# Kernel tuning notes

Hardware: AMD Instinct MI355X
Metric: run time of the kernel (lower is better)

## Reference

```python
import jax, jax.numpy as jnp
import numpy as np

LN_EPS = 1e-5

def setup_inputs() -> dict:
    key = jax.random.key(0)
    k1, k2, k3, k4, k5, k6 = jax.random.split(key, 6)
    N, D, E_DIM = 100000, 512, 512
    M, n_edges = 500000, 100000
    z_nodes = jax.random.normal(k1, (N, D), dtype=jnp.float32)
    member_idx = jax.random.randint(k2, (M,), 0, N, dtype=jnp.int32)
    seg_ids = jnp.sort(jax.random.randint(k3, (M,), 0, n_edges, dtype=jnp.int32))
    # aggregator params: Linear(D -> E_DIM), LayerNorm(E_DIM)
    W = jax.random.normal(k4, (D, E_DIM), dtype=jnp.float32) / np.sqrt(D)
    b = jax.random.normal(k5, (E_DIM,), dtype=jnp.float32) * 0.01
    gamma = jnp.ones((E_DIM,), dtype=jnp.float32)
    beta = jnp.zeros((E_DIM,), dtype=jnp.float32)
    return {"z_nodes": z_nodes, "W": W, "b": b, "gamma": gamma, "beta": beta,
            "member_idx": member_idx, "seg_ids": seg_ids, "n_edges": n_edges}

def reference(z_nodes, W, b, gamma, beta, member_idx, seg_ids, n_edges):
    # ragged gather + per-edge mean pool (segment mean)
    gathered = z_nodes[member_idx]                                   # [M, D]
    sums = jax.ops.segment_sum(gathered, seg_ids, num_segments=n_edges)  # [E, D]
    counts = jax.ops.segment_sum(jnp.ones((member_idx.shape[0],), dtype=z_nodes.dtype),
                                 seg_ids, num_segments=n_edges)      # [E]
    mean = sums / jnp.maximum(counts, 1.0)[:, None]                  # [E, D]
    # Linear -> LayerNorm -> GELU (torch GELU default is exact erf form)
    h = mean @ W + b                                                 # [E, edge_dim]
    mu = jnp.mean(h, axis=-1, keepdims=True)
    var = jnp.mean(jnp.square(h - mu), axis=-1, keepdims=True)
    h = (h - mu) * jax.lax.rsqrt(var + LN_EPS) * gamma + beta
    return jax.nn.gelu(h, approximate=False)
```

## Files before the change

### kernel.cpp

```cpp
#include <hip/hip_runtime.h>
#include <hip/hip_bf16.h>
#include <stdint.h>


typedef __attribute__((ext_vector_type(8))) short short8;
typedef __attribute__((ext_vector_type(4))) float f32x4;
typedef __attribute__((ext_vector_type(4))) float float4v;
typedef __attribute__((ext_vector_type(4))) unsigned short u16x4;

__device__ __forceinline__ unsigned short f2bf(float f) {
  __hip_bfloat16 h = __float2bfloat16(f);
  return __builtin_bit_cast(unsigned short, h);
}
__device__ __forceinline__ float bf2f(unsigned short u) {
  __hip_bfloat16 h = __builtin_bit_cast(__hip_bfloat16, u);
  return __bfloat162float(h);
}

__device__ __forceinline__ void gld_lds16(const void* g, void* l) {
  __builtin_amdgcn_global_load_lds(
      (const __attribute__((address_space(1))) uint32_t*)g,
      (__attribute__((address_space(3))) uint32_t*)l, 16, 0, 0);
}

__global__ void k_zero(int* __restrict__ beg, int* __restrict__ end_, int E) {
  int i = blockIdx.x * 256 + threadIdx.x;
  if (i < E) { beg[i] = 0; end_[i] = 0; }
}

__global__ void k_bounds(const int* __restrict__ seg, int* __restrict__ beg,
                         int* __restrict__ end_, int M) {
  int i = blockIdx.x * 256 + threadIdx.x;
  if (i >= M) return;
  int s = seg[i];
  if (i == 0 || seg[i - 1] != s) beg[s] = i;
  if (i == M - 1 || seg[i + 1] != s) end_[s] = i + 1;
}

__global__ void k_wsplit(const float* __restrict__ W, unsigned short* __restrict__ Whi,
                         unsigned short* __restrict__ Wlo) {
  int t = blockIdx.x * 256 + threadIdx.x;
  if (t >= 512 * 512) return;
  int k = t >> 9, c = t & 511;
  float w = W[t];
  unsigned short hi = f2bf(w);
  unsigned short lo = f2bf(w - bf2f(hi));
  int o = (k >> 3) * 4096 + c * 8 + (k & 7);
  Whi[o] = hi;
  Wlo[o] = lo;
}

__global__ void k_mean(const float* __restrict__ z, const int* __restrict__ midx,
                       const int* __restrict__ beg, const int* __restrict__ end_,
                       unsigned short* a16) {
  const int e = blockIdx.x;
  const int t = threadIdx.x;
  const int b = beg[e], en = end_[e];
  float4v acc = {0.f, 0.f, 0.f, 0.f};
  for (int m = b; m < en; ++m) {
    const int r = midx[m];
    const float4v v = *(const float4v*)(z + (size_t)r * 512 + t * 4);
    acc.x += v.x; acc.y += v.y; acc.z += v.z; acc.w += v.w;
  }
  const int cnt = en - b;
  const float den = (float)(cnt > 0 ? cnt : 1);
  float m0 = acc.x / den, m1 = acc.y / den, m2 = acc.z / den, m3 = acc.w / den;
  u16x4 hi, lo;
  hi.x = f2bf(m0); lo.x = f2bf(m0 - bf2f(hi.x));
  hi.y = f2bf(m1); lo.y = f2bf(m1 - bf2f(hi.y));
  hi.z = f2bf(m2); lo.z = f2bf(m2 - bf2f(hi.z));
  hi.w = f2bf(m3); lo.w = f2bf(m3 - bf2f(hi.w));
  *(u16x4*)(a16 + (size_t)e * 1024 + t * 4) = hi;
  *(u16x4*)(a16 + (size_t)e * 1024 + 512 + t * 4) = lo;
}

#define KSTEPS 48

__launch_bounds__(256, 2)
__global__ void k_gemm(const unsigned short* a16,
                       const unsigned short* __restrict__ Whi,
                       const unsigned short* __restrict__ Wlo,
                       const float* __restrict__ bias, const float* __restrict__ gamma,
                       const float* __restrict__ beta, float* out, int E) {
  __shared__ short lA[2][64 * 32];
  __shared__ short lB[2][4 * 512 * 8];
  __shared__ float lRed[64 * 4];
  __shared__ float lMu[64], lRs[64];

  const int t = threadIdx.x;
  const int w = t >> 6, l = t & 63;
  const int g = l >> 4, l15 = l & 15;
  const int cw = w * 128;
  const int e0 = blockIdx.x * 64;

  f32x4 acc[4][8];
#pragma unroll
  for (int mf = 0; mf < 4; ++mf)
#pragma unroll
    for (int nf = 0; nf < 8; ++nf) acc[mf][nf] = (f32x4){0.f, 0.f, 0.f, 0.f};

  auto stage = [&](int s) {
    const int p = s >> 4, kt = s & 15, buf = s & 1;
    const int poff = (p == 1) ? 512 : 0;
    const unsigned short* Bs = (p == 2) ? Wlo : Whi;
    {
      const int row = t >> 2, cd = t & 3;
      const int cs = cd ^ ((row >> 1) & 3);
      int rsrc = e0 + row;
      if (rsrc > E - 1) rsrc = E - 1;
      gld_lds16(a16 + (size_t)rsrc * 1024 + poff + kt * 32 + cs * 8,
                &lA[buf][w * 512]);
    }
    const unsigned short* gb = Bs + (size_t)kt * 16384;
#pragma unroll
    for (int i = 0; i < 8; ++i) {
      gld_lds16(gb + (size_t)(i * 256 + t) * 8, &lB[buf][(i * 256 + w * 64) * 8]);
    }
  };

  stage(0);
  for (int s = 0; s < KSTEPS; ++s) {
    __syncthreads();
    if (s + 1 < KSTEPS) stage(s + 1);
    const int buf = s & 1;
    short8 af[4];
#pragma unroll
    for (int mf = 0; mf < 4; ++mf) {
      const int R = 16 * mf + l15;
      const int cc = g ^ ((R >> 1) & 3);
      af[mf] = *(const short8*)&lA[buf][R * 32 + cc * 8];
    }
#pragma unroll
    for (int nf = 0; nf < 8; ++nf) {
      const short8 bf = *(const short8*)&lB[buf][(g * 512 + cw + 16 * nf + l15) * 8];
#pragma unroll
      for (int mf = 0; mf < 4; ++mf)
        acc[mf][nf] = __builtin_amdgcn_mfma_f32_16x16x32_bf16(af[mf], bf, acc[mf][nf], 0, 0, 0);
    }
  }
  __syncthreads();

  float bia[8], gam[8], bet[8];
#pragma unroll
  for (int nf = 0; nf < 8; ++nf) {
    const int col = cw + 16 * nf + l15;
    bia[nf] = bias[col]; gam[nf] = gamma[col]; bet[nf] = beta[col];
  }
#pragma unroll
  for (int mf = 0; mf < 4; ++mf)
#pragma unroll
    for (int nf = 0; nf < 8; ++nf)
#pragma unroll
      for (int r = 0; r < 4; ++r) acc[mf][nf][r] += bia[nf];

  float s_[4][4];
#pragma unroll
  for (int mf = 0; mf < 4; ++mf)
#pragma unroll
    for (int r = 0; r < 4; ++r) {
      float v = 0.f;
#pragma unroll
      for (int nf = 0; nf < 8; ++nf) v += acc[mf][nf][r];
      v += __shfl_xor(v, 1); v += __shfl_xor(v, 2);
      v += __shfl_xor(v, 4); v += __shfl_xor(v, 8);
      s_[mf][r] = v;
    }
  if (l15 == 0) {
#pragma unroll
    for (int mf = 0; mf < 4; ++mf)
#pragma unroll
      for (int r = 0; r < 4; ++r) lRed[(16 * mf + 4 * g + r) * 4 + w] = s_[mf][r];
  }
  __syncthreads();
  if (t < 64) lMu[t] = (lRed[t * 4] + lRed[t * 4 + 1] + lRed[t * 4 + 2] + lRed[t * 4 + 3]) * (1.f / 512.f);
  __syncthreads();

  float mu_[4][4];
#pragma unroll
  for (int mf = 0; mf < 4; ++mf)
#pragma unroll
    for (int r = 0; r < 4; ++r) mu_[mf][r] = lMu[16 * mf + 4 * g + r];
#pragma unroll
  for (int mf = 0; mf < 4; ++mf)
#pragma unroll
    for (int r = 0; r < 4; ++r) {
      float v = 0.f;
#pragma unroll
      for (int nf = 0; nf < 8; ++nf) {
        const float d = acc[mf][nf][r] - mu_[mf][r];
        v += d * d;
      }
      v += __shfl_xor(v, 1); v += __shfl_xor(v, 2);
      v += __shfl_xor(v, 4); v += __shfl_xor(v, 8);
      s_[mf][r] = v;
    }
  if (l15 == 0) {
#pragma unroll
    for (int mf = 0; mf < 4; ++mf)
#pragma unroll
      for (int r = 0; r < 4; ++r) lRed[(16 * mf + 4 * g + r) * 4 + w] = s_[mf][r];
  }
  __syncthreads();
  if (t < 64) {
    const float sse = lRed[t * 4] + lRed[t * 4 + 1] + lRed[t * 4 + 2] + lRed[t * 4 + 3];
    lRs[t] = rsqrtf(sse * (1.f / 512.f) + 1e-5f);
  }
  __syncthreads();

#pragma unroll
  for (int mf = 0; mf < 4; ++mf)
#pragma unroll
    for (int r = 0; r < 4; ++r) {
      const int row = 16 * mf + 4 * g + r;
      const int er = e0 + row;
      if (er >= E) continue;
      const float mu = lMu[row], rs = lRs[row];
#pragma unroll
      for (int nf = 0; nf < 8; ++nf) {
        const int col = cw + 16 * nf + l15;
        const float x = (acc[mf][nf][r] - mu) * rs * gam[nf] + bet[nf];
        const float y = 0.5f * x * (1.f + erff(x * 0.70710678118654752f));
        out[(size_t)er * 512 + col] = y;
      }
    }
}

extern "C" void kernel_launch(void* const* d_in, const int* in_sizes, int n_in,
                              void* d_out, int out_size, void* d_ws, size_t ws_size,
                              hipStream_t stream) {
  const float* z = (const float*)d_in[0];
  const float* W = (const float*)d_in[1];
  const float* bias = (const float*)d_in[2];
  const float* gamma = (const float*)d_in[3];
  const float* beta = (const float*)d_in[4];
  const int* midx = (const int*)d_in[5];
  const int* seg = (const int*)d_in[6];
  const int M = in_sizes[5];
  const int E = out_size / 512;

  char* ws = (char*)d_ws;
  size_t off = 0;
  auto alloc = [&](size_t bytes) {
    void* p = ws + off;
    off = (off + bytes + 255) & ~(size_t)255;
    return p;
  };
  int* beg = (int*)alloc((size_t)E * 4);
  int* end_ = (int*)alloc((size_t)E * 4);
  unsigned short* Whi = (unsigned short*)alloc((size_t)512 * 512 * 2);
  unsigned short* Wlo = (unsigned short*)alloc((size_t)512 * 512 * 2);
  (void)ws_size; (void)n_in;

  unsigned short* a16 = (unsigned short*)d_out;

  k_zero<<<(E + 255) / 256, 256, 0, stream>>>(beg, end_, E);
  k_bounds<<<(M + 255) / 256, 256, 0, stream>>>(seg, beg, end_, M);
  k_wsplit<<<(512 * 512 + 255) / 256, 256, 0, stream>>>(W, Whi, Wlo);
  k_mean<<<E, 128, 0, stream>>>(z, midx, beg, end_, a16);
  k_gemm<<<(E + 63) / 64, 256, 0, stream>>>(a16, Whi, Wlo, bias, gamma, beta,
                                            (float*)d_out, E);
}
```

Before: 803.6 us.

## Unroll gather in mean kernel and load GEMM operands directly from global

The mean kernel now gives each edge one wavefront, handles four members per iteration with two float4 loads per lane, and multiplies by a reciprocal instead of dividing. This is meant to keep more gather loads in flight. The GEMM drops its LDS double-buffered staging and reads A and B fragments straight from global/L2 into registers, removing barriers and LDS traffic. The cost is that operand reuse through shared memory is lost, so B is fetched separately by every wave and block and more cache bandwidth is needed.

```diff
diff --git a/kernel.cpp b/kernel.cpp
--- a/kernel.cpp
+++ b/kernel.cpp
@@ -5,7 +5,6 @@
 
 typedef __attribute__((ext_vector_type(8))) short short8;
 typedef __attribute__((ext_vector_type(4))) float f32x4;
-typedef __attribute__((ext_vector_type(4))) float float4v;
 typedef __attribute__((ext_vector_type(4))) unsigned short u16x4;
 
 __device__ __forceinline__ unsigned short f2bf(float f) {
@@ -15,12 +14,6 @@
 __device__ __forceinline__ float bf2f(unsigned short u) {
   __hip_bfloat16 h = __builtin_bit_cast(__hip_bfloat16, u);
   return __bfloat162float(h);
-}
-
-__device__ __forceinline__ void gld_lds16(const void* g, void* l) {
-  __builtin_amdgcn_global_load_lds(
-      (const __attribute__((address_space(1))) uint32_t*)g,
-      (__attribute__((address_space(3))) uint32_t*)l, 16, 0, 0);
 }
 
 __global__ void k_zero(int* __restrict__ beg, int* __restrict__ end_, int E) {
@@ -52,29 +45,47 @@
 
 __global__ void k_mean(const float* __restrict__ z, const int* __restrict__ midx,
                        const int* __restrict__ beg, const int* __restrict__ end_,
-                       unsigned short* a16) {
-  const int e = blockIdx.x;
-  const int t = threadIdx.x;
+                       unsigned short* a16, int E) {
+  const int w = threadIdx.x >> 6, l = threadIdx.x & 63;
+  const int e = blockIdx.x * 4 + w;
+  if (e >= E) return;
   const int b = beg[e], en = end_[e];
-  float4v acc = {0.f, 0.f, 0.f, 0.f};
-  for (int m = b; m < en; ++m) {
+  const float* zl = z + l * 4;
+  f32x4 a0 = {0.f, 0.f, 0.f, 0.f}, a1 = {0.f, 0.f, 0.f, 0.f};
+  int m = b;
+  for (; m + 4 <= en; m += 4) {
+    const int r0 = midx[m], r1 = midx[m + 1], r2 = midx[m + 2], r3 = midx[m + 3];
+    const f32x4 u0 = *(const f32x4*)(zl + (size_t)r0 * 512);
+    const f32x4 u1 = *(const f32x4*)(zl + (size_t)r0 * 512 + 256);
+    const f32x4 v0 = *(const f32x4*)(zl + (size_t)r1 * 512);
+    const f32x4 v1 = *(const f32x4*)(zl + (size_t)r1 * 512 + 256);
+    const f32x4 s0 = *(const f32x4*)(zl + (size_t)r2 * 512);
+    const f32x4 s1 = *(const f32x4*)(zl + (size_t)r2 * 512 + 256);
+    const f32x4 t0 = *(const f32x4*)(zl + (size_t)r3 * 512);
+    const f32x4 t1 = *(const f32x4*)(zl + (size_t)r3 * 512 + 256);
+    a0 += u0; a1 += u1; a0 += v0; a1 += v1;
+    a0 += s0; a1 += s1; a0 += t0; a1 += t1;
+  }
+  for (; m < en; ++m) {
     const int r = midx[m];
-    const float4v v = *(const float4v*)(z + (size_t)r * 512 + t * 4);
-    acc.x += v.x; acc.y += v.y; acc.z += v.z; acc.w += v.w;
+    a0 += *(const f32x4*)(zl + (size_t)r * 512);
+    a1 += *(const f32x4*)(zl + (size_t)r * 512 + 256);
   }
   const int cnt = en - b;
-  const float den = (float)(cnt > 0 ? cnt : 1);
-  float m0 = acc.x / den, m1 = acc.y / den, m2 = acc.z / den, m3 = acc.w / den;
-  u16x4 hi, lo;
-  hi.x = f2bf(m0); lo.x = f2bf(m0 - bf2f(hi.x));
-  hi.y = f2bf(m1); lo.y = f2bf(m1 - bf2f(hi.y));
-  hi.z = f2bf(m2); lo.z = f2bf(m2 - bf2f(hi.z));
-  hi.w = f2bf(m3); lo.w = f2bf(m3 - bf2f(hi.w));
-  *(u16x4*)(a16 + (size_t)e * 1024 + t * 4) = hi;
-  *(u16x4*)(a16 + (size_t)e * 1024 + 512 + t * 4) = lo;
-}
-
-#define KSTEPS 48
+  const float den = 1.f / (float)(cnt > 0 ? cnt : 1);
+  u16x4 h0, l0, h1, l1;
+#pragma unroll
+  for (int j = 0; j < 4; ++j) {
+    const float m0 = a0[j] * den, m1 = a1[j] * den;
+    h0[j] = f2bf(m0); l0[j] = f2bf(m0 - bf2f(h0[j]));
+    h1[j] = f2bf(m1); l1[j] = f2bf(m1 - bf2f(h1[j]));
+  }
+  unsigned short* rowp = a16 + (size_t)e * 1024;
+  *(u16x4*)(rowp + l * 4) = h0;
+  *(u16x4*)(rowp + 256 + l * 4) = h1;
+  *(u16x4*)(rowp + 512 + l * 4) = l0;
+  *(u16x4*)(rowp + 768 + l * 4) = l1;
+}
 
 __launch_bounds__(256, 2)
 __global__ void k_gemm(const unsigned short* a16,
@@ -82,8 +93,6 @@
                        const unsigned short* __restrict__ Wlo,
                        const float* __restrict__ bias, const float* __restrict__ gamma,
                        const float* __restrict__ beta, float* out, int E) {
-  __shared__ short lA[2][64 * 32];
-  __shared__ short lB[2][4 * 512 * 8];
   __shared__ float lRed[64 * 4];
   __shared__ float lMu[64], lRs[64];
 
@@ -93,52 +102,41 @@
   const int cw = w * 128;
   const int e0 = blockIdx.x * 64;
 
+  const unsigned short* pA[4];
+#pragma unroll
+  for (int mf = 0; mf < 4; ++mf) {
+    int R = e0 + 16 * mf + l15;
+    if (R > E - 1) R = E - 1;
+    pA[mf] = a16 + (size_t)R * 1024 + g * 8;
+  }
+  const size_t bOff = (size_t)g * 4096 + (size_t)(cw + l15) * 8;
+
   f32x4 acc[4][8];
 #pragma unroll
   for (int mf = 0; mf < 4; ++mf)
 #pragma unroll
     for (int nf = 0; nf < 8; ++nf) acc[mf][nf] = (f32x4){0.f, 0.f, 0.f, 0.f};
 
-  auto stage = [&](int s) {
-    const int p = s >> 4, kt = s & 15, buf = s & 1;
+  for (int p = 0; p < 3; ++p) {
+    const unsigned short* pB = ((p == 2) ? Wlo : Whi) + bOff;
     const int poff = (p == 1) ? 512 : 0;
-    const unsigned short* Bs = (p == 2) ? Wlo : Whi;
-    {
-      const int row = t >> 2, cd = t & 3;
-      const int cs = cd ^ ((row >> 1) & 3);
-      int rsrc = e0 + row;
-      if (rsrc > E - 1) rsrc = E - 1;
-      gld_lds16(a16 + (size_t)rsrc * 1024 + poff + kt * 32 + cs * 8,
-                &lA[buf][w * 512]);
-    }
-    const unsigned short* gb = Bs + (size_t)kt * 16384;
-#pragma unroll
-    for (int i = 0; i < 8; ++i) {
-      gld_lds16(gb + (size_t)(i * 256 + t) * 8, &lB[buf][(i * 256 + w * 64) * 8]);
-    }
-  };
-
-  stage(0);
-  for (int s = 0; s < KSTEPS; ++s) {
-    __syncthreads();
-    if (s + 1 < KSTEPS) stage(s + 1);
-    const int buf = s & 1;
-    short8 af[4];
-#pragma unroll
-    for (int mf = 0; mf < 4; ++mf) {
-      const int R = 16 * mf + l15;
-      const int cc = g ^ ((R >> 1) & 3);
-      af[mf] = *(const short8*)&lA[buf][R * 32 + cc * 8];
-    }
-#pragma unroll
-    for (int nf = 0; nf < 8; ++nf) {
-      const short8 bf = *(const short8*)&lB[buf][(g * 512 + cw + 16 * nf + l15) * 8];
+#pragma unroll 2
+    for (int kt = 0; kt < 16; ++kt) {
+      short8 af[4];
 #pragma unroll
       for (int mf = 0; mf < 4; ++mf)
-        acc[mf][nf] = __builtin_amdgcn_mfma_f32_16x16x32_bf16(af[mf], bf, acc[mf][nf], 0, 0, 0);
-    }
-  }
-  __syncthreads();
+        af[mf] = *(const short8*)(pA[mf] + poff + kt * 32);
+      short8 bf[8];
+#pragma unroll
+      for (int nf = 0; nf < 8; ++nf)
+        bf[nf] = *(const short8*)(pB + (size_t)kt * 16384 + nf * 128);
+#pragma unroll
+      for (int nf = 0; nf < 8; ++nf)
+#pragma unroll
+        for (int mf = 0; mf < 4; ++mf)
+          acc[mf][nf] = __builtin_amdgcn_mfma_f32_16x16x32_bf16(af[mf], bf[nf], acc[mf][nf], 0, 0, 0);
+    }
+  }
 
   float bia[8], gam[8], bet[8];
 #pragma unroll
@@ -256,7 +254,7 @@
   k_zero<<<(E + 255) / 256, 256, 0, stream>>>(beg, end_, E);
   k_bounds<<<(M + 255) / 256, 256, 0, stream>>>(seg, beg, end_, M);
   k_wsplit<<<(512 * 512 + 255) / 256, 256, 0, stream>>>(W, Whi, Wlo);
-  k_mean<<<E, 128, 0, stream>>>(z, midx, beg, end_, a16);
+  k_mean<<<(E + 3) / 4, 256, 0, stream>>>(z, midx, beg, end_, a16, E);
   k_gemm<<<(E + 63) / 64, 256, 0, stream>>>(a16, Whi, Wlo, bias, gamma, beta,
                                             (float*)d_out, E);
 }
```

After: 873.8 us. 1.09x slower.

## Fuse segment-mean gather into GEMM kernel and drop A low-part split

Applied to the files above, without the earlier changes.

The gather/mean pooling is moved into the GEMM kernel. Each block computes the 64 edge means directly into a swizzled LDS tile, so the bf16 hi/lo activation buffer is no longer written to and read back from global memory. The A low-part pass is dropped, which cuts the K steps from 48 to 32 (A_hi*W_hi + A_hi*W_lo only). This lowers accuracy of the emulated fp32 GEMM, and the larger LDS footprint limits occupancy to one block per CU, so the gather latency may be less well hidden.

```diff
diff --git a/kernel.cpp b/kernel.cpp
--- a/kernel.cpp
+++ b/kernel.cpp
@@ -4,9 +4,8 @@
 
 
 typedef __attribute__((ext_vector_type(8))) short short8;
+typedef __attribute__((ext_vector_type(8))) unsigned short ushort8;
 typedef __attribute__((ext_vector_type(4))) float f32x4;
-typedef __attribute__((ext_vector_type(4))) float float4v;
-typedef __attribute__((ext_vector_type(4))) unsigned short u16x4;
 
 __device__ __forceinline__ unsigned short f2bf(float f) {
   __hip_bfloat16 h = __float2bfloat16(f);
@@ -50,40 +49,17 @@
   Wlo[o] = lo;
 }
 
-__global__ void k_mean(const float* __restrict__ z, const int* __restrict__ midx,
-                       const int* __restrict__ beg, const int* __restrict__ end_,
-                       unsigned short* a16) {
-  const int e = blockIdx.x;
-  const int t = threadIdx.x;
-  const int b = beg[e], en = end_[e];
-  float4v acc = {0.f, 0.f, 0.f, 0.f};
-  for (int m = b; m < en; ++m) {
-    const int r = midx[m];
-    const float4v v = *(const float4v*)(z + (size_t)r * 512 + t * 4);
-    acc.x += v.x; acc.y += v.y; acc.z += v.z; acc.w += v.w;
-  }
-  const int cnt = en - b;
-  const float den = (float)(cnt > 0 ? cnt : 1);
-  float m0 = acc.x / den, m1 = acc.y / den, m2 = acc.z / den, m3 = acc.w / den;
-  u16x4 hi, lo;
-  hi.x = f2bf(m0); lo.x = f2bf(m0 - bf2f(hi.x));
-  hi.y = f2bf(m1); lo.y = f2bf(m1 - bf2f(hi.y));
-  hi.z = f2bf(m2); lo.z = f2bf(m2 - bf2f(hi.z));
-  hi.w = f2bf(m3); lo.w = f2bf(m3 - bf2f(hi.w));
-  *(u16x4*)(a16 + (size_t)e * 1024 + t * 4) = hi;
-  *(u16x4*)(a16 + (size_t)e * 1024 + 512 + t * 4) = lo;
-}
-
-#define KSTEPS 48
-
-__launch_bounds__(256, 2)
-__global__ void k_gemm(const unsigned short* a16,
-                       const unsigned short* __restrict__ Whi,
-                       const unsigned short* __restrict__ Wlo,
-                       const float* __restrict__ bias, const float* __restrict__ gamma,
-                       const float* __restrict__ beta, float* out, int E) {
-  __shared__ short lA[2][64 * 32];
-  __shared__ short lB[2][4 * 512 * 8];
+#define KSTEPS 32
+
+__launch_bounds__(256, 1)
+__global__ void k_fused(const float* __restrict__ z, const int* __restrict__ midx,
+                        const int* __restrict__ beg, const int* __restrict__ end_,
+                        const unsigned short* __restrict__ Whi,
+                        const unsigned short* __restrict__ Wlo,
+                        const float* __restrict__ bias, const float* __restrict__ gamma,
+                        const float* __restrict__ beta, float* __restrict__ out, int E) {
+  __shared__ short lA[64 * 512];
+  __shared__ short lB[2][16384];
   __shared__ float lRed[64 * 4];
   __shared__ float lMu[64], lRs[64];
 
@@ -93,6 +69,40 @@
   const int cw = w * 128;
   const int e0 = blockIdx.x * 64;
 
+  for (int i = 0; i < 16; ++i) {
+    const int row = w * 16 + i;
+    const int e = e0 + row;
+    f32x4 a0 = {0.f, 0.f, 0.f, 0.f}, a1 = {0.f, 0.f, 0.f, 0.f};
+    if (e < E) {
+      const int b = beg[e], en = end_[e];
+      int m = b;
+      for (; m + 2 <= en; m += 2) {
+        const int r0 = midx[m], r1 = midx[m + 1];
+        const float* p0 = z + (size_t)r0 * 512 + 8 * l;
+        const float* p1 = z + (size_t)r1 * 512 + 8 * l;
+        const f32x4 u0 = *(const f32x4*)p0, u1 = *(const f32x4*)(p0 + 4);
+        const f32x4 v0 = *(const f32x4*)p1, v1 = *(const f32x4*)(p1 + 4);
+        a0 += u0; a1 += u1; a0 += v0; a1 += v1;
+      }
+      if (m < en) {
+        const int r0 = midx[m];
+        const float* p0 = z + (size_t)r0 * 512 + 8 * l;
+        a0 += *(const f32x4*)p0;
+        a1 += *(const f32x4*)(p0 + 4);
+      }
+      const int cnt = en - b;
+      const float den = 1.f / (float)(cnt > 0 ? cnt : 1);
+      a0 *= den; a1 *= den;
+    }
+    ushort8 hv;
+#pragma unroll
+    for (int j = 0; j < 4; ++j) {
+      hv[j] = f2bf(a0[j]);
+      hv[4 + j] = f2bf(a1[j]);
+    }
+    *(ushort8*)&lA[row * 512 + ((l ^ (row & 7)) * 8)] = hv;
+  }
+
   f32x4 acc[4][8];
 #pragma unroll
   for (int mf = 0; mf < 4; ++mf)
@@ -101,34 +111,22 @@
 
   auto stage = [&](int s) {
     const int p = s >> 4, kt = s & 15, buf = s & 1;
-    const int poff = (p == 1) ? 512 : 0;
-    const unsigned short* Bs = (p == 2) ? Wlo : Whi;
-    {
-      const int row = t >> 2, cd = t & 3;
-      const int cs = cd ^ ((row >> 1) & 3);
-      int rsrc = e0 + row;
-      if (rsrc > E - 1) rsrc = E - 1;
-      gld_lds16(a16 + (size_t)rsrc * 1024 + poff + kt * 32 + cs * 8,
-                &lA[buf][w * 512]);
-    }
-    const unsigned short* gb = Bs + (size_t)kt * 16384;
-#pragma unroll
-    for (int i = 0; i < 8; ++i) {
+    const unsigned short* gb = ((p == 1) ? Wlo : Whi) + (size_t)kt * 16384;
+#pragma unroll
+    for (int i = 0; i < 8; ++i)
       gld_lds16(gb + (size_t)(i * 256 + t) * 8, &lB[buf][(i * 256 + w * 64) * 8]);
-    }
   };
 
   stage(0);
   for (int s = 0; s < KSTEPS; ++s) {
     __syncthreads();
     if (s + 1 < KSTEPS) stage(s + 1);
-    const int buf = s & 1;
+    const int buf = s & 1, kt = s & 15;
     short8 af[4];
 #pragma unroll
     for (int mf = 0; mf < 4; ++mf) {
       const int R = 16 * mf + l15;
-      const int cc = g ^ ((R >> 1) & 3);
-      af[mf] = *(const short8*)&lA[buf][R * 32 + cc * 8];
+      af[mf] = *(const short8*)&lA[R * 512 + (((kt * 4 + g) ^ (R & 7)) * 8)];
     }
 #pragma unroll
     for (int nf = 0; nf < 8; ++nf) {
@@ -251,12 +249,9 @@
   unsigned short* Wlo = (unsigned short*)alloc((size_t)512 * 512 * 2);
   (void)ws_size; (void)n_in;
 
-  unsigned short* a16 = (unsigned short*)d_out;
-
   k_zero<<<(E + 255) / 256, 256, 0, stream>>>(beg, end_, E);
   k_bounds<<<(M + 255) / 256, 256, 0, stream>>>(seg, beg, end_, M);
   k_wsplit<<<(512 * 512 + 255) / 256, 256, 0, stream>>>(W, Whi, Wlo);
-  k_mean<<<E, 128, 0, stream>>>(z, midx, beg, end_, a16);
-  k_gemm<<<(E + 63) / 64, 256, 0, stream>>>(a16, Whi, Wlo, bias, gamma, beta,
-                                            (float*)d_out, E);
-}
+  k_fused<<<(E + 63) / 64, 256, 0, stream>>>(z, midx, beg, end_, Whi, Wlo, bias,
+                                             gamma, beta, (float*)d_out, E);
+}
```

After: 925.8 us. +15.2%, slower.
